# Performance work log

Measured on AMD Instinct MI355X. Metric: run time of the kernel, lower is better.

## Reference

```python
import jax, jax.numpy as jnp
import numpy as np

HEIGHT = 8  # init kwarg: output crop height
B, J, C, HIMG, WIMG = 8, 64, 32, 256, 256


def _make_boxes():
    rng = np.random.default_rng(0)
    left = rng.uniform(0.0, 40.0, (B, J))
    bw = rng.uniform(16.0, 200.0, (B, J))
    top = rng.uniform(0.0, 200.0, (B, J))
    bh = rng.uniform(8.0, 32.0, (B, J))
    theta = rng.uniform(-0.5, 0.5, (B, J))  # unused by the original forward
    return np.stack([left, top, left + bw, top + bh, theta], axis=-1).astype(np.float32)


def _box_widths(boxes_np):
    # torch: width = int(aspect * height), truncation (values are positive)
    bw = boxes_np[..., 2] - boxes_np[..., 0]
    bh = boxes_np[..., 3] - boxes_np[..., 1]
    return ((bw / bh) * HEIGHT).astype(np.int32)  # [B, J]


def setup_inputs() -> dict:
    key = jax.random.key(0)
    image = jax.random.normal(key, (B, C, HIMG, WIMG), dtype=jnp.float32)
    boxes = jnp.asarray(_make_boxes())
    return {"image": image, "boxes": boxes}


def reference(image, boxes):
    # Per-box widths are integer (shape-determining) constants, taken from concrete box data.
    boxes_np = np.asarray(jax.device_get(boxes))
    widths_np = _box_widths(boxes_np)          # [B, J] ints >= 2
    max_w = int(widths_np.max())
    widths = jnp.asarray(widths_np)

    dt = boxes.dtype
    base_w = boxes[..., 2] - boxes[..., 0]      # [B, J]
    base_h = boxes[..., 3] - boxes[..., 1]
    each_w = base_w / (widths.astype(dt) - 1)   # [B, J]
    each_h = base_h / (HEIGHT - 1)

    # Sampling grids: xx [B,J,Wm], yy [B,J,Hh]
    xx = jnp.arange(max_w, dtype=dt)[None, None, :] * each_w[..., None] + boxes[..., 0:1]
    yy = jnp.arange(HEIGHT, dtype=dt)[None, None, :] * each_h[..., None] + boxes[..., 1:2]

    def interp_one_image(img, x, y):
        # img [C,Hi,Wi], x [J,Wm], y [J,Hh] -> [C,J,Hh,Wm]
        x0 = jnp.clip(jnp.floor(x).astype(jnp.int32), 0, WIMG - 1)
        x1 = jnp.clip(jnp.floor(x).astype(jnp.int32) + 1, 0, WIMG - 1)
        y0 = jnp.clip(jnp.floor(y).astype(jnp.int32), 0, HIMG - 1)
        y1 = jnp.clip(jnp.floor(y).astype(jnp.int32) + 1, 0, HIMG - 1)
        # gathers: [C, J, Hh, Wm]
        ia = img[:, y0[:, :, None], x0[:, None, :]]
        ib = img[:, y1[:, :, None], x0[:, None, :]]
        ic = img[:, y0[:, :, None], x1[:, None, :]]
        idd = img[:, y1[:, :, None], x1[:, None, :]]
        x0f, x1f = x0.astype(dt), x1.astype(dt)
        y0f, y1f = y0.astype(dt), y1.astype(dt)
        wa = (x1f - x)[:, None, :] * (y1f - y)[:, :, None]  # [J,Hh,Wm]
        wb = (x1f - x)[:, None, :] * (y - y0f)[:, :, None]
        wc = (x - x0f)[:, None, :] * (y1f - y)[:, :, None]
        wd = (x - x0f)[:, None, :] * (y - y0f)[:, :, None]
        return ia * wa[None] + ib * wb[None] + ic * wc[None] + idd * wd[None]

    res = jax.vmap(interp_one_image)(image, xx, yy)      # [B,C,J,Hh,Wm]
    res = jnp.transpose(res, (0, 2, 1, 3, 4))            # [B,J,C,Hh,Wm]

    mask = (jnp.arange(max_w)[None, None, :] < widths[..., None]).astype(jnp.uint8)  # [B,J,Wm]
    res = res * mask[:, :, None, None, :].astype(res.dtype)  # zero-pad beyond each box width
    return res, mask
```

## Files before the change

kernel.cpp:

```cpp
#include <hip/hip_runtime.h>

#define HIMG 256
#define WIMG 256
#define CCH  32
#define JBOX 64
#define BIMG 8
#define HGT  8
#define NBUF 3
#define WCOLS 52

typedef __attribute__((address_space(3))) float lds_f;
typedef const __attribute__((address_space(1))) float glb_f;

__global__ __launch_bounds__(256, 6) void roi_kernel(
    const float* __restrict__ img,
    const float* __restrict__ boxes,
    float* __restrict__ res,
    float* __restrict__ mask,
    int max_w)
{
    __shared__ float sbuf[4][NBUF][2][208];

    const int d    = blockIdx.x;
    const int b    = d & 7;
    const int seq  = d >> 3;
    const int cg   = seq >> 6;
    const int j    = seq & 63;
    const int bj   = b * JBOX + j;
    const int tid  = threadIdx.x;
    const int wv   = tid >> 6;
    const int lane = tid & 63;
    const int c    = cg * 4 + wv;

    const float left = boxes[bj * 5 + 0];
    const float top  = boxes[bj * 5 + 1];
    const float bw   = boxes[bj * 5 + 2] - left;
    const float bh   = boxes[bj * 5 + 3] - top;

    const int   width  = (int)(bw / bh * 8.0f);
    const float each_w = bw / ((float)width - 1.0f);
    const float each_h = bh / 7.0f;

    const int xs  = max((int)floorf(left), 0);
    const int xs4 = xs & ~3;

    int   lxk[4];
    float wx0k[4], wx1k[4];
    #pragma unroll
    for (int k = 0; k < 4; ++k) {
        if (64 * k < max_w) {
            const int   i  = 64 * k + lane;
            const float x  = __fadd_rn(__fmul_rn((float)i, each_w), left);
            const int   xf = (int)floorf(x);
            const int   x0 = min(max(xf, 0), WIMG - 1);
            wx1k[k] = (float)(x0 + 1) - x;
            wx0k[k] = x - (float)x0;
            lxk[k]  = min(max(x0 - xs4, 0), 206);
        }
    }

    const float* chbase = img + (size_t)(b * CCH + c) * (HIMG * WIMG);

    auto dma = [&](int h, int bf) {
        const float yh  = __fadd_rn(__fmul_rn((float)h, each_h), top);
        const int   yfl = (int)floorf(yh);
        const int   ya  = min(max(yfl,     0), HIMG - 1);
        const int   yb  = min(max(yfl + 1, 0), HIMG - 1);
        if (lane < WCOLS) {
            const float* s0 = chbase + (size_t)ya * WIMG + xs4 + 4 * lane;
            const float* s1 = chbase + (size_t)yb * WIMG + xs4 + 4 * lane;
            __builtin_amdgcn_global_load_lds((glb_f*)s0, (lds_f*)&sbuf[wv][bf][0][0], 16, 0, 0);
            __builtin_amdgcn_global_load_lds((glb_f*)s1, (lds_f*)&sbuf[wv][bf][1][0], 16, 0, 0);
        }
    };

    auto consume = [&](int h, int bf, float4& A) {
        const float yh  = __fadd_rn(__fmul_rn((float)h, each_h), top);
        const int   yfl = (int)floorf(yh);
        const int   ya  = min(max(yfl,     0), HIMG - 1);
        const int   yb  = min(max(yfl + 1, 0), HIMG - 1);
        const float wy1 = (float)yb - yh;
        const float wy0 = yh - (float)ya;
        float vals[4] = {0.0f, 0.0f, 0.0f, 0.0f};
        #pragma unroll
        for (int k = 0; k < 4; ++k) {
            if (64 * k < max_w) {
                const float v00 = sbuf[wv][bf][0][lxk[k]];
                const float v01 = sbuf[wv][bf][0][lxk[k] + 1];
                const float v10 = sbuf[wv][bf][1][lxk[k]];
                const float v11 = sbuf[wv][bf][1][lxk[k] + 1];
                const float wa  = wx1k[k] * wy1;
                const float wb_ = wx1k[k] * wy0;
                const float wc_ = wx0k[k] * wy1;
                const float wd_ = wx0k[k] * wy0;
                vals[k] = v00 * wa + v10 * wb_ + v01 * wc_ + v11 * wd_;
            }
        }
        A.x = vals[0]; A.y = vals[1]; A.z = vals[2]; A.w = vals[3];
    };

    float4 a0, a1, a2, a3, a4, a5, a6, a7;

    dma(0, 0);
    dma(1, 1);
    dma(2, 2);
    __builtin_amdgcn_sched_barrier(0);

#define STEP(H, BF, WN, A)                                                    \
    do {                                                                      \
        asm volatile("s_waitcnt vmcnt(" #WN ")" ::: "memory");                \
        __builtin_amdgcn_sched_barrier(0);                                    \
        consume(H, BF, A);                                                    \
               \
        asm volatile("s_waitcnt lgkmcnt(0)" ::: "memory");                    \
        __builtin_amdgcn_sched_barrier(0);                                    \
        if ((H) + 3 < HGT) dma((H) + 3, BF);                                  \
    } while (0)

    STEP(0, 0, 4, a0);
    STEP(1, 1, 4, a1);
    STEP(2, 2, 4, a2);
    STEP(3, 0, 4, a3);
    STEP(4, 1, 4, a4);
    STEP(5, 2, 4, a5);
    STEP(6, 0, 2, a6);
    STEP(7, 1, 0, a7);
#undef STEP

    float* rb = res + ((size_t)(bj * CCH + c) * HGT) * (size_t)max_w;

#define STORE_H(H, A)                                                         \
    do {                                                                      \
        const float vals[4] = {A.x, A.y, A.z, A.w};                           \
        _Pragma("unroll")                                                     \
        for (int k = 0; k < 4; ++k) {                                         \
            const int ii = 64 * k + lane;                                     \
            if (ii < max_w)                                                   \
                rb[(size_t)(H) * max_w + ii] = (ii < width) ? vals[k] : 0.0f; \
        }                                                                     \
    } while (0)

    STORE_H(0, a0); STORE_H(1, a1); STORE_H(2, a2); STORE_H(3, a3);
    STORE_H(4, a4); STORE_H(5, a5); STORE_H(6, a6); STORE_H(7, a7);
#undef STORE_H

    if (c == 0) {
        #pragma unroll
        for (int k = 0; k < 4; ++k) {
            const int ii = 64 * k + lane;
            if (ii < max_w)
                mask[(size_t)bj * max_w + ii] = (ii < width) ? 1.0f : 0.0f;
        }
    }
}

extern "C" void kernel_launch(void* const* d_in, const int* in_sizes, int n_in,
                              void* d_out, int out_size, void* d_ws, size_t ws_size,
                              hipStream_t stream) {
    const float* img   = (const float*)d_in[0];
    const float* boxes = (const float*)d_in[1];
    float* out = (float*)d_out;

    const int per_w = BIMG * JBOX * CCH * HGT + BIMG * JBOX;
    const int max_w = out_size / per_w;

    float* res  = out;
    float* mask = out + (size_t)BIMG * JBOX * CCH * HGT * max_w;

    const int blocks = BIMG * JBOX * CCH / 4;
    roi_kernel<<<blocks, 256, 0, stream>>>(img, boxes, res, mask, max_w);
}
```

Before: 152.9 us.

## Stage output tile in LDS and write it with contiguous float4 stores

Each wave now writes its interpolated 8 x max_w output tile into a per-wave LDS staging buffer. It then streams the whole contiguous per-channel output block to global memory with 16-byte vector stores instead of scalar per-row stores. The aim is fewer, wider, fully coalesced writes. In exchange, LDS use per block grows by about 26 KB and the launch-bounds occupancy hint drops from 6 to 3 blocks. The float4 store assumes the output base is 16-byte aligned, which holds only if 8*max_w*4 bytes is a multiple of 16. It also assumes max_w is at most 208.

```diff
diff --git a/kernel.cpp b/kernel.cpp
--- a/kernel.cpp
+++ b/kernel.cpp
@@ -8,11 +8,12 @@
 #define HGT  8
 #define NBUF 3
 #define WCOLS 52
+#define OSW  208
 
 typedef __attribute__((address_space(3))) float lds_f;
 typedef const __attribute__((address_space(1))) float glb_f;
 
-__global__ __launch_bounds__(256, 6) void roi_kernel(
+__global__ __launch_bounds__(256, 3) void roi_kernel(
     const float* __restrict__ img,
     const float* __restrict__ boxes,
     float* __restrict__ res,
@@ -20,6 +21,7 @@
     int max_w)
 {
     __shared__ float sbuf[4][NBUF][2][208];
+    __shared__ float ostage[4][HGT][OSW];
 
     const int d    = blockIdx.x;
     const int b    = d & 7;
@@ -74,17 +76,17 @@
         }
     };
 
-    auto consume = [&](int h, int bf, float4& A) {
+    auto consume = [&](int h, int bf) {
         const float yh  = __fadd_rn(__fmul_rn((float)h, each_h), top);
         const int   yfl = (int)floorf(yh);
         const int   ya  = min(max(yfl,     0), HIMG - 1);
         const int   yb  = min(max(yfl + 1, 0), HIMG - 1);
         const float wy1 = (float)yb - yh;
         const float wy0 = yh - (float)ya;
-        float vals[4] = {0.0f, 0.0f, 0.0f, 0.0f};
         #pragma unroll
         for (int k = 0; k < 4; ++k) {
             if (64 * k < max_w) {
+                const int   ii  = 64 * k + lane;
                 const float v00 = sbuf[wv][bf][0][lxk[k]];
                 const float v01 = sbuf[wv][bf][0][lxk[k] + 1];
                 const float v10 = sbuf[wv][bf][1][lxk[k]];
@@ -93,58 +95,57 @@
                 const float wb_ = wx1k[k] * wy0;
                 const float wc_ = wx0k[k] * wy1;
                 const float wd_ = wx0k[k] * wy0;
-                vals[k] = v00 * wa + v10 * wb_ + v01 * wc_ + v11 * wd_;
+                const float val = v00 * wa + v10 * wb_ + v01 * wc_ + v11 * wd_;
+                ostage[wv][h][ii] = (ii < width) ? val : 0.0f;
             }
         }
-        A.x = vals[0]; A.y = vals[1]; A.z = vals[2]; A.w = vals[3];
     };
-
-    float4 a0, a1, a2, a3, a4, a5, a6, a7;
 
     dma(0, 0);
     dma(1, 1);
     dma(2, 2);
     __builtin_amdgcn_sched_barrier(0);
 
-#define STEP(H, BF, WN, A)                                                    \
+#define STEP(H, BF, WN)                                                       \
     do {                                                                      \
         asm volatile("s_waitcnt vmcnt(" #WN ")" ::: "memory");                \
         __builtin_amdgcn_sched_barrier(0);                                    \
-        consume(H, BF, A);                                                    \
+        consume(H, BF);                                                       \
                \
         asm volatile("s_waitcnt lgkmcnt(0)" ::: "memory");                    \
         __builtin_amdgcn_sched_barrier(0);                                    \
         if ((H) + 3 < HGT) dma((H) + 3, BF);                                  \
     } while (0)
 
-    STEP(0, 0, 4, a0);
-    STEP(1, 1, 4, a1);
-    STEP(2, 2, 4, a2);
-    STEP(3, 0, 4, a3);
-    STEP(4, 1, 4, a4);
-    STEP(5, 2, 4, a5);
-    STEP(6, 0, 2, a6);
-    STEP(7, 1, 0, a7);
+    STEP(0, 0, 4);
+    STEP(1, 1, 4);
+    STEP(2, 2, 4);
+    STEP(3, 0, 4);
+    STEP(4, 1, 4);
+    STEP(5, 2, 4);
+    STEP(6, 0, 2);
+    STEP(7, 1, 0);
 #undef STEP
 
-    float* rb = res + ((size_t)(bj * CCH + c) * HGT) * (size_t)max_w;
+    float* jobbase = res + (size_t)(bj * CCH + c) * (size_t)(HGT * max_w);
+    const int m  = max_w;
+    const int m2 = 2 * m, m4 = 4 * m;
+    for (int g = lane; g < 2 * m; g += 64) {
+        int p = 4 * g;
+        int h = 0;
+        if (p >= m4) { h  = 4; p -= m4; }
+        if (p >= m2) { h += 2; p -= m2; }
+        if (p >= m)  { h += 1; p -= m; }
+        const int c1 = (p + 1 >= m), c2 = (p + 2 >= m), c3 = (p + 3 >= m);
+        float4 v;
+        v.x = ostage[wv][h][p];
+        v.y = ostage[wv][h + c1][p + 1 - (c1 ? m : 0)];
+        v.z = ostage[wv][h + c2][p + 2 - (c2 ? m : 0)];
+        v.w = ostage[wv][h + c3][p + 3 - (c3 ? m : 0)];
+        *reinterpret_cast<float4*>(jobbase + (size_t)4 * g) = v;
+    }
 
-#define STORE_H(H, A)                                                         \
-    do {                                                                      \
-        const float vals[4] = {A.x, A.y, A.z, A.w};                           \
-        _Pragma("unroll")                                                     \
-        for (int k = 0; k < 4; ++k) {                                         \
-            const int ii = 64 * k + lane;                                     \
-            if (ii < max_w)                                                   \
-                rb[(size_t)(H) * max_w + ii] = (ii < width) ? vals[k] : 0.0f; \
-        }                                                                     \
-    } while (0)
-
-    STORE_H(0, a0); STORE_H(1, a1); STORE_H(2, a2); STORE_H(3, a3);
-    STORE_H(4, a4); STORE_H(5, a5); STORE_H(6, a6); STORE_H(7, a7);
-#undef STORE_H
-
-    if (c == 0) {
+    if (cg == 0 && wv == 0) {
         #pragma unroll
         for (int k = 0; k < 4; ++k) {
             const int ii = 64 * k + lane;
```

Result: slower. 171.3 us (+12.1%).
